# Optimization experiments

Hardware: AMD Instinct MI355X
Metric: run time of the kernel (lower is better)

The kernel has to match this reference:

```python
import jax, jax.numpy as jnp
import numpy as np

FILTER_SIZE = 7
STOPBAND_REL = 2.0 ** 0.3


def _kaiser_beta(a):
    if a > 50.0:
        return 0.1102 * (a - 8.7)
    if a > 21.0:
        return 0.5842 * (a - 21.0) ** 0.4 + 0.07886 * (a - 21.0)
    return 0.0


def design_up_filter(in_size):
    # Reproduces design_lowpass_filter_dct(numtaps=15, cutoff=in_size/2,
    # width=2*in_half_width, fs=2*in_size) = scipy.signal.firwin w/ kaiser window.
    fs = 2.0 * in_size
    cutoff = in_size / 2.0
    half_width = cutoff * (STOPBAND_REL - 1.0)  # max(stopband, fs_in/2) - cutoff
    width = 2.0 * half_width
    numtaps = FILTER_SIZE * 2 + 1  # up_taps = 7*2 -> made odd -> 15
    nyq = fs / 2.0
    atten = 2.285 * (numtaps - 1) * np.pi * (width / nyq) + 7.95  # kaiser_atten
    beta = _kaiser_beta(atten)
    m = np.arange(numtaps) - (numtaps - 1) / 2.0
    c = cutoff / nyq
    h = c * np.sinc(c * m) * np.kaiser(numtaps, beta)
    h = h / h.sum()  # firwin scale=True at DC
    f = h.astype(np.float32)
    return f / (f[numtaps // 2:].sum() * 2.0)


def _dct_mats(N):
    # torch_dct norm=None DCT-II: D[k,n] = 2*cos(pi*k*(2n+1)/(2N)); exact inverse
    # via row orthogonality: Dinv[n,k] = D[k,n] * s[k], s[0]=1/(4N), s[k>0]=1/(2N).
    n = np.arange(N)
    k = n[:, None]
    D = 2.0 * np.cos(np.pi * (2 * n + 1) * k / (2.0 * N))
    s = np.full(N, 1.0 / (2.0 * N))
    s[0] = 1.0 / (4.0 * N)
    Dinv = (D * s[:, None]).T
    return jnp.asarray(D, jnp.float32), jnp.asarray(Dinv, jnp.float32)


def upsample2d_dct(x, f):
    B, C, H, W = x.shape
    p = FILTER_SIZE // 2  # padding = 3
    taps = f.shape[0]
    # reflect pad (padx0=padx1=pady0=pady1=p)
    xp = jnp.pad(x, ((0, 0), (0, 0), (p, p), (p, p)), mode='reflect')
    Hp, Wp = H + 2 * p, W + 2 * p
    Hu, Wu = 2 * Hp, 2 * Wp
    # zero-stuff upsample by 2 (sample at even positions)
    xu = jnp.zeros((B, C, Hu, Wu), x.dtype).at[:, :, ::2, ::2].set(xp)
    # gain = up_factor**2 = 4; f *= gain**(f.ndim/2) = 2; flip (symmetric filter)
    g = (f * 2.0)[::-1]
    half = g[taps // 2:]  # 8 taps incl. center
    nh = half.shape[0]
    f1 = jnp.zeros((Hu, Wu), jnp.float32).at[0, :nh].set(half)  # row filter
    f2 = jnp.zeros((Hu, Wu), jnp.float32).at[:nh, 0].set(half)  # col filter
    Dh, Dhi = _dct_mats(Hu)
    Dw, Dwi = _dct_mats(Wu)
    dct2 = lambda a: Dh @ a @ Dw.T  # DCT-II along both spatial dims
    Xf = dct2(xu)
    F1 = dct2(f1)
    F2 = dct2(f2)
    y = (Dhi @ (F1 * F2 * Xf) @ Dwi.T) / np.float32(np.sqrt(np.pi * 5.0))
    # crop the padding back out and fold the up-factor into spatial dims
    y = y.reshape(B, C, Hp, 2, Wp, 2)[:, :, p:Hp - p, :, p:Wp - p, :]
    return y.reshape(B, C, 2 * H, 2 * W)


def setup_inputs() -> dict:
    key = jax.random.key(0)
    B, C, H, W = 4, 32, 256, 256
    x = jax.random.normal(key, (B, C, H, W), dtype=jnp.float32)
    up_filter = jnp.asarray(design_up_filter(W))  # deterministic 15-tap buffer
    return {"x": x, "up_filter": up_filter}


def reference(x, up_filter):
    return upsample2d_dct(x, up_filter)
```

## Files before the change

kernel.cpp:

```cpp
#include <hip/hip_runtime.h>

#define BLOCK 256
#define TILE 64
#define PR 40
#define HW 256
#define OWID 512

typedef float f32x2 __attribute__((ext_vector_type(2)));
typedef float f32x4 __attribute__((ext_vector_type(4)));

__global__ __launch_bounds__(BLOCK) void up2d_kernel(
    const float* __restrict__ x,
    const float* __restrict__ f,
    float* __restrict__ out)
{
    __shared__ float P[PR][42];
    __shared__ float T[TILE][42];

    const int tid = threadIdx.x;

    const int L = blockIdx.x;
    const int orig = ((L & 7) << 10) | (L >> 3);
    const int bc   = orig >> 6;
    const int tile = orig & 63;

    const int ty = (tile >> 3) * TILE;
    const int tx = (tile & 7) * TILE;
    const int ry0 = (ty >> 1) - 1;
    const int rx0 = (tx >> 1) - 1;

    float g[9];
    g[0] = 4.0f * f[7];
#pragma unroll
    for (int k = 1; k <= 7; ++k) g[k] = 2.0f * (f[7 + k] + f[6 + k]);
    g[8] = 2.0f * f[14];

    float wE[9], wO[8];
#pragma unroll
    for (int q = 0; q < 9; ++q) { int d = 8 - 2 * q; wE[q] = g[d < 0 ? -d : d]; }
#pragma unroll
    for (int q = 0; q < 8; ++q) { int d = 7 - 2 * q; wO[q] = g[d < 0 ? -d : d]; }
    const float g7 = g[7], g8 = g[8];

    const float* xc = x + (size_t)bc * (HW * HW);
#pragma unroll
    for (int it = 0; it < 7; ++it) {
        int w = it * BLOCK + tid;
        if (w < PR * PR) {
            int r = w / PR;
            int c = w - r * PR;
            int gr = ry0 + r, gc = rx0 + c;
            int sr = gr - 3; sr = sr < 0 ? -sr : sr; sr = sr >= HW ? 2 * HW - 2 - sr : sr;
            int sc = gc - 3; sc = sc < 0 ? -sc : sc; sc = sc >= HW ? 2 * HW - 2 - sc : sc;
            float v = xc[sr * HW + sc];
            if ((unsigned)gr >= 262u || (unsigned)gc >= 262u) v = 0.0f;
            P[c][r] = v;
        }
    }
    __syncthreads();

#pragma unroll
    for (int it = 0; it < 3; ++it) {
        int w = it * BLOCK + tid;
        if (w < 640) {
            int k2 = w / PR;
            int c  = w - k2 * PR;
            f32x2 b0 = *reinterpret_cast<const f32x2*>(&P[c][2 * k2]);
            f32x2 b1 = *reinterpret_cast<const f32x2*>(&P[c][2 * k2 + 2]);
            f32x2 b2 = *reinterpret_cast<const f32x2*>(&P[c][2 * k2 + 4]);
            f32x2 b3 = *reinterpret_cast<const f32x2*>(&P[c][2 * k2 + 6]);
            f32x2 b4 = *reinterpret_cast<const f32x2*>(&P[c][2 * k2 + 8]);
            float v[10] = {b0.x, b0.y, b1.x, b1.y, b2.x,
                           b2.y, b3.x, b3.y, b4.x, b4.y};
#pragma unroll
            for (int t = 0; t < 2; ++t) {
                float aE = 0.0f, aO = 0.0f;
#pragma unroll
                for (int q = 0; q < 9; ++q) aE = fmaf(wE[q], v[t + q], aE);
#pragma unroll
                for (int q = 0; q < 8; ++q) aO = fmaf(wO[q], v[t + 1 + q], aO);
                int k = 2 * k2 + t;
                if (ty == 0 && k == 0)    { aE += g7 * v[1]; aO += g8 * v[1]; }
                if (ty == 448 && k == 31) { aO += g8 * v[8]; }
                T[2 * k][c]     = aE;
                T[2 * k + 1][c] = aO;
            }
        }
    }
    __syncthreads();

    const float inv_s = 0.25231325f;
    float* oc = out + (size_t)bc * ((size_t)OWID * OWID);
#pragma unroll
    for (int it = 0; it < 4; ++it) {
        int w = it * BLOCK + tid;
        int orow = w >> 4;
        int q4 = w & 15;
        float v[10];
#pragma unroll
        for (int q = 0; q < 10; ++q) v[q] = T[orow][2 * q4 + q];
        float r0 = 0.f, r1 = 0.f, r2 = 0.f, r3 = 0.f;
#pragma unroll
        for (int q = 0; q < 9; ++q) { r0 = fmaf(wE[q], v[q], r0); r2 = fmaf(wE[q], v[q + 1], r2); }
#pragma unroll
        for (int q = 0; q < 8; ++q) { r1 = fmaf(wO[q], v[q + 1], r1); r3 = fmaf(wO[q], v[q + 2], r3); }
        if (tx == 0 && q4 == 0)    { r0 += g7 * T[orow][1]; r1 += g8 * T[orow][1]; }
        if (tx == 448 && q4 == 15) { r3 += g8 * T[orow][38]; }
        f32x4 o4 = {r0 * inv_s, r1 * inv_s, r2 * inv_s, r3 * inv_s};
        __builtin_nontemporal_store(o4,
            reinterpret_cast<f32x4*>(&oc[(size_t)(ty + orow) * OWID + tx + 4 * q4]));
    }
}

extern "C" void kernel_launch(void* const* d_in, const int* in_sizes, int n_in,
                              void* d_out, int out_size, void* d_ws, size_t ws_size,
                              hipStream_t stream) {
    const float* x = (const float*)d_in[0];
    const float* f = (const float*)d_in[1];
    float* out = (float*)d_out;
    up2d_kernel<<<dim3(8192), BLOCK, 0, stream>>>(x, f, out);
}
```

Measured before the change: 34.97 us.

## Switch to full-width row-strip tiles for separable upsample filter

Each block now handles a full-width strip of 8 output rows (264 padded input columns by 12 rows) instead of a 64x64 output tile. This removes the horizontal halo recomputation and makes each row's global stores contiguous across 2 KB. The horizontal pass reads LDS with vectorized f32x2 loads, and the output stores drop the nontemporal hint for plain stores. The trade-offs: the vertical halo ratio is now higher (12 input rows for 4 useful), and only 264 of 512 threads' worth of work is active in the vertical pass.

Result: slower. 36.03 us (+3.0%).

```diff
diff --git a/kernel.cpp b/kernel.cpp
--- a/kernel.cpp
+++ b/kernel.cpp
@@ -1,10 +1,12 @@
 #include <hip/hip_runtime.h>
 
 #define BLOCK 256
-#define TILE 64
-#define PR 40
 #define HW 256
 #define OWID 512
+#define PCOLS 264
+#define PROWS 12
+#define PPITCH 14
+#define TPITCH 266
 
 typedef float f32x2 __attribute__((ext_vector_type(2)));
 typedef float f32x4 __attribute__((ext_vector_type(4)));
@@ -14,20 +16,16 @@
     const float* __restrict__ f,
     float* __restrict__ out)
 {
-    __shared__ float P[PR][42];
-    __shared__ float T[TILE][42];
+    __shared__ float P[PCOLS][PPITCH];
+    __shared__ float T[8][TPITCH];
 
     const int tid = threadIdx.x;
 
     const int L = blockIdx.x;
     const int orig = ((L & 7) << 10) | (L >> 3);
-    const int bc   = orig >> 6;
-    const int tile = orig & 63;
-
-    const int ty = (tile >> 3) * TILE;
-    const int tx = (tile & 7) * TILE;
-    const int ry0 = (ty >> 1) - 1;
-    const int rx0 = (tx >> 1) - 1;
+    const int bc = orig >> 6;
+    const int rt = orig & 63;
+    const int ry0 = 4 * rt - 1;
 
     float g[9];
     g[0] = 4.0f * f[7];
@@ -44,12 +42,13 @@
 
     const float* xc = x + (size_t)bc * (HW * HW);
 #pragma unroll
-    for (int it = 0; it < 7; ++it) {
+    for (int it = 0; it < 13; ++it) {
         int w = it * BLOCK + tid;
-        if (w < PR * PR) {
-            int r = w / PR;
-            int c = w - r * PR;
-            int gr = ry0 + r, gc = rx0 + c;
+        if (w < PROWS * PCOLS) {
+            int r = w / PCOLS;
+            int c = w - r * PCOLS;
+            int gr = ry0 + r;
+            int gc = c - 1;
             int sr = gr - 3; sr = sr < 0 ? -sr : sr; sr = sr >= HW ? 2 * HW - 2 - sr : sr;
             int sc = gc - 3; sc = sc < 0 ? -sc : sc; sc = sc >= HW ? 2 * HW - 2 - sc : sc;
             float v = xc[sr * HW + sc];
@@ -60,55 +59,55 @@
     __syncthreads();
 
 #pragma unroll
-    for (int it = 0; it < 3; ++it) {
-        int w = it * BLOCK + tid;
-        if (w < 640) {
-            int k2 = w / PR;
-            int c  = w - k2 * PR;
-            f32x2 b0 = *reinterpret_cast<const f32x2*>(&P[c][2 * k2]);
-            f32x2 b1 = *reinterpret_cast<const f32x2*>(&P[c][2 * k2 + 2]);
-            f32x2 b2 = *reinterpret_cast<const f32x2*>(&P[c][2 * k2 + 4]);
-            f32x2 b3 = *reinterpret_cast<const f32x2*>(&P[c][2 * k2 + 6]);
-            f32x2 b4 = *reinterpret_cast<const f32x2*>(&P[c][2 * k2 + 8]);
-            float v[10] = {b0.x, b0.y, b1.x, b1.y, b2.x,
-                           b2.y, b3.x, b3.y, b4.x, b4.y};
+    for (int it = 0; it < 2; ++it) {
+        int c = it * BLOCK + tid;
+        if (c < PCOLS) {
+            f32x2 b0 = *reinterpret_cast<const f32x2*>(&P[c][0]);
+            f32x2 b1 = *reinterpret_cast<const f32x2*>(&P[c][2]);
+            f32x2 b2 = *reinterpret_cast<const f32x2*>(&P[c][4]);
+            f32x2 b3 = *reinterpret_cast<const f32x2*>(&P[c][6]);
+            f32x2 b4 = *reinterpret_cast<const f32x2*>(&P[c][8]);
+            f32x2 b5 = *reinterpret_cast<const f32x2*>(&P[c][10]);
+            float v[12] = {b0.x, b0.y, b1.x, b1.y, b2.x, b2.y,
+                           b3.x, b3.y, b4.x, b4.y, b5.x, b5.y};
 #pragma unroll
-            for (int t = 0; t < 2; ++t) {
+            for (int t = 0; t < 4; ++t) {
                 float aE = 0.0f, aO = 0.0f;
 #pragma unroll
                 for (int q = 0; q < 9; ++q) aE = fmaf(wE[q], v[t + q], aE);
 #pragma unroll
                 for (int q = 0; q < 8; ++q) aO = fmaf(wO[q], v[t + 1 + q], aO);
-                int k = 2 * k2 + t;
-                if (ty == 0 && k == 0)    { aE += g7 * v[1]; aO += g8 * v[1]; }
-                if (ty == 448 && k == 31) { aO += g8 * v[8]; }
-                T[2 * k][c]     = aE;
-                T[2 * k + 1][c] = aO;
+                if (rt == 0 && t == 0)  { aE += g7 * v[1]; aO += g8 * v[1]; }
+                if (rt == 63 && t == 3) { aO += g8 * v[10]; }
+                T[2 * t][c]     = aE;
+                T[2 * t + 1][c] = aO;
             }
         }
     }
     __syncthreads();
 
     const float inv_s = 0.25231325f;
-    float* oc = out + (size_t)bc * ((size_t)OWID * OWID);
+    float* oc = out + (size_t)bc * ((size_t)OWID * OWID) + (size_t)(8 * rt) * OWID;
 #pragma unroll
     for (int it = 0; it < 4; ++it) {
         int w = it * BLOCK + tid;
-        int orow = w >> 4;
-        int q4 = w & 15;
+        int orow = w >> 7;
+        int q4 = w & 127;
         float v[10];
 #pragma unroll
-        for (int q = 0; q < 10; ++q) v[q] = T[orow][2 * q4 + q];
+        for (int q = 0; q < 5; ++q) {
+            f32x2 b = *reinterpret_cast<const f32x2*>(&T[orow][2 * q4 + 2 * q]);
+            v[2 * q] = b.x; v[2 * q + 1] = b.y;
+        }
         float r0 = 0.f, r1 = 0.f, r2 = 0.f, r3 = 0.f;
 #pragma unroll
         for (int q = 0; q < 9; ++q) { r0 = fmaf(wE[q], v[q], r0); r2 = fmaf(wE[q], v[q + 1], r2); }
 #pragma unroll
         for (int q = 0; q < 8; ++q) { r1 = fmaf(wO[q], v[q + 1], r1); r3 = fmaf(wO[q], v[q + 2], r3); }
-        if (tx == 0 && q4 == 0)    { r0 += g7 * T[orow][1]; r1 += g8 * T[orow][1]; }
-        if (tx == 448 && q4 == 15) { r3 += g8 * T[orow][38]; }
+        if (q4 == 0)   { r0 += g7 * T[orow][1];   r1 += g8 * T[orow][1]; }
+        if (q4 == 127) { r3 += g8 * T[orow][262]; }
         f32x4 o4 = {r0 * inv_s, r1 * inv_s, r2 * inv_s, r3 * inv_s};
-        __builtin_nontemporal_store(o4,
-            reinterpret_cast<f32x4*>(&oc[(size_t)(ty + orow) * OWID + tx + 4 * q4]));
+        *reinterpret_cast<f32x4*>(&oc[(size_t)orow * OWID + 4 * q4]) = o4;
     }
 }
 
```
